# Kernel tuning notes

Measured on AMD Instinct MI355X. Metric: run time of the kernel, lower is better.

## Reference

```python
import jax, jax.numpy as jnp
import numpy as np

N_NODES = 50000
N_EDGES = 800000
N_GRAPHS = 256
C_FEAT = 108
MLP_DIM = 88
OUT_DIM = 100


def setup_inputs() -> dict:
    key = jax.random.key(0)
    ks = jax.random.split(key, 12)
    x = jax.random.normal(ks[0], (N_NODES, C_FEAT), dtype=jnp.float32)
    edge_index = jax.random.randint(ks[1], (2, N_EDGES), 0, N_NODES, dtype=jnp.int64)
    batch = jnp.sort(jax.random.randint(ks[2], (N_NODES,), 0, N_GRAPHS, dtype=jnp.int64))

    def glorot(k, shape):
        fan_in, fan_out = shape
        s = jnp.sqrt(2.0 / (fan_in + fan_out))
        return jax.random.normal(k, shape, dtype=jnp.float32) * s

    return {
        "x": x,
        "edge_index": edge_index,
        "batch": batch,
        # SAGEConv layer 1: lin_l (neighbors, has bias), lin_r (root, no bias)
        "W1l": glorot(ks[3], (C_FEAT, MLP_DIM)),
        "W1r": glorot(ks[4], (C_FEAT, MLP_DIM)),
        "b1": jnp.zeros((MLP_DIM,), jnp.float32),
        "W2l": glorot(ks[5], (MLP_DIM, MLP_DIM)),
        "W2r": glorot(ks[6], (MLP_DIM, MLP_DIM)),
        "b2": jnp.zeros((MLP_DIM,), jnp.float32),
        "W3l": glorot(ks[7], (MLP_DIM, MLP_DIM)),
        "W3r": glorot(ks[8], (MLP_DIM, MLP_DIM)),
        "b3": jnp.zeros((MLP_DIM,), jnp.float32),
        "Wlin": glorot(ks[9], (MLP_DIM, OUT_DIM)),
        "blin": jnp.zeros((OUT_DIM,), jnp.float32),
    }


def _sage_conv(x, src, dst, Wl, Wr, b):
    """PyG SAGEConv(aggr='mean'): out = lin_l(mean_j x_j) + lin_r(x)."""
    n = x.shape[0]
    msg = x[src]  # [E, d] gather from source nodes
    agg = jax.ops.segment_sum(msg, dst, num_segments=n)  # [N, d]
    cnt = jax.ops.segment_sum(jnp.ones((src.shape[0],), x.dtype), dst, num_segments=n)
    agg = agg / jnp.maximum(cnt, 1.0)[:, None]  # scatter-mean
    return agg @ Wl + b + x @ Wr


def reference(x, edge_index, batch, W1l, W1r, b1, W2l, W2r, b2, W3l, W3r, b3, Wlin, blin):
    src, dst = edge_index[0], edge_index[1]
    h = jax.nn.relu(_sage_conv(x, src, dst, W1l, W1r, b1))
    h = jax.nn.relu(_sage_conv(h, src, dst, W2l, W2r, b2))
    h = jax.nn.relu(_sage_conv(h, src, dst, W3l, W3r, b3))
    pooled = jax.ops.segment_sum(h, batch, num_segments=N_GRAPHS)  # global_add_pool
    return pooled @ Wlin + blin  # [n_graphs, 100]
```

## Files before the change

kernel.cpp:

```cpp
#include <hip/hip_runtime.h>
#include <hip/hip_fp16.h>

#define NN 50000
#define NG 256
#define CF 108
#define MD 88
#define OD 100
#define F2 44
#define HP 96
#define HP2 48
#define YLS 96
#define K1P 128
#define NSB 196
#define SBCAP 5120
#define TILE 2048
#define NCH 12

typedef _Float16 f16x8 __attribute__((ext_vector_type(8)));
typedef float f32x4 __attribute__((ext_vector_type(4)));


__global__ __launch_bounds__(256) void bin_kernel(const int* __restrict__ edge, int E,
                                                  int* __restrict__ sbcur,
                                                  unsigned* __restrict__ sbrec) {
    __shared__ int bcnt[NSB], boff[NSB], bfill[NSB], gbase[NSB];
    __shared__ int sc[256];
    __shared__ unsigned stag[TILE];
    __shared__ unsigned char stagbin[TILE];
    const int tid = threadIdx.x;
    const int t0  = blockIdx.x * TILE;
    const int tcnt = min(TILE, E - t0);

    for (int i = tid; i < NSB; i += 256) bcnt[i] = 0;
    __syncthreads();

    unsigned recs[TILE / 256];
    int      bins[TILE / 256];
    #pragma unroll
    for (int j = 0; j < TILE / 256; ++j) {
        const int e = t0 + j * 256 + tid;
        bins[j] = -1;
        if (e < E) {
            const int dst = edge[E + e], src = edge[e];
            bins[j] = dst >> 8;
            recs[j] = ((unsigned)src << 8) | (unsigned)(dst & 255);
            atomicAdd(&bcnt[bins[j]], 1);
        }
    }
    __syncthreads();

    sc[tid] = (tid < NSB) ? bcnt[tid] : 0;
    __syncthreads();
    for (int d = 1; d < 256; d <<= 1) {
        int v = (tid >= d) ? sc[tid - d] : 0;
        __syncthreads();
        sc[tid] += v;
        __syncthreads();
    }
    if (tid < NSB) {
        boff[tid]  = sc[tid] - bcnt[tid];
        bfill[tid] = sc[tid] - bcnt[tid];
        if (bcnt[tid] > 0) gbase[tid] = atomicAdd(&sbcur[tid], bcnt[tid]);
    }
    __syncthreads();

    #pragma unroll
    for (int j = 0; j < TILE / 256; ++j) {
        if (bins[j] >= 0) {
            int pos = atomicAdd(&bfill[bins[j]], 1);
            stag[pos]    = recs[j];
            stagbin[pos] = (unsigned char)bins[j];
        }
    }
    __syncthreads();

    for (int i = tid; i < tcnt; i += 256) {
        const int b   = stagbin[i];
        const int rel = i - boff[b];
        const int gp  = gbase[b] + rel;
        if (gp < SBCAP) sbrec[(size_t)b * SBCAP + gp] = stag[i];
    }
}


__global__ __launch_bounds__(256) void csr256_kernel(const unsigned* __restrict__ sbrec,
                                                     const int* __restrict__ sbcur,
                                                     int* __restrict__ csr,
                                                     int2* __restrict__ off2, int N) {
    __shared__ int hist[256], base[256], offc[256], sc[256];
    const int b = blockIdx.x, tid = threadIdx.x;
    const int cnt = min(sbcur[b], SBCAP);
    const unsigned* rec = sbrec + (size_t)b * SBCAP;

    hist[tid] = 0;
    __syncthreads();
    for (int r = tid; r < cnt; r += 256) atomicAdd(&hist[rec[r] & 255u], 1);
    __syncthreads();

    sc[tid] = hist[tid];
    __syncthreads();
    for (int d = 1; d < 256; d <<= 1) {
        int v = (tid >= d) ? sc[tid - d] : 0;
        __syncthreads();
        sc[tid] += v;
        __syncthreads();
    }
    base[tid] = sc[tid] - hist[tid];
    offc[tid] = base[tid];
    __syncthreads();

    for (int r = tid; r < cnt; r += 256) {
        const unsigned u = rec[r];
        const int dl = (int)(u & 255u);
        const int pos = atomicAdd(&offc[dl], 1);
        csr[(size_t)b * SBCAP + pos] = (int)(u >> 8);
    }
    __syncthreads();

    const int n = b * 256 + tid;
    if (n < N) off2[n] = make_int2(b * SBCAP + base[tid], hist[tid]);
}


__global__ void convx_kernel(const float* __restrict__ x, _Float16* __restrict__ xh, int N) {
    int i = blockIdx.x * blockDim.x + threadIdx.x;
    if (i >= N * K1P) return;
    int n = i >> 7, k = i & (K1P - 1);
    xh[i] = (k < CF) ? (_Float16)x[n * CF + k] : (_Float16)0.f;
}


__global__ void build_wct_all(const float* __restrict__ W1l, const float* __restrict__ W1r,
                              const float* __restrict__ W2l, const float* __restrict__ W2r,
                              const float* __restrict__ W3l, const float* __restrict__ W3r,
                              _Float16* __restrict__ Wct1, _Float16* __restrict__ Wct23) {
    const int n1 = 176 * K1P;
    const int n2 = 176 * HP;
    int idx = blockIdx.x * blockDim.x + threadIdx.x;
    if (idx < n1) {
        int c = idx / K1P, k = idx - c * K1P;
        float v = (k < CF) ? ((c < MD) ? W1l[k * MD + c] : W1r[k * MD + (c - MD)]) : 0.f;
        Wct1[idx] = (_Float16)v;
    } else if (idx < n1 + 2 * n2) {
        int j = idx - n1;
        const float* Wl = (j < n2) ? W2l : W3l;
        const float* Wr = (j < n2) ? W2r : W3r;
        int jj = (j < n2) ? j : j - n2;
        int c = jj / HP, k = jj - c * HP;
        float v = (k < MD) ? ((c < MD) ? Wl[k * MD + c] : Wr[k * MD + (c - MD)]) : 0.f;
        Wct23[j] = (_Float16)v;
    }
}


template <int KPAD>
__global__ __launch_bounds__(256) void gemm_mfma_kernel(const _Float16* __restrict__ Ah,
                                                        const _Float16* __restrict__ Wct,
                                                        const float* __restrict__ bias,
                                                        _Float16* __restrict__ yl,
                                                        _Float16* __restrict__ yr, int N) {
    const int wave = threadIdx.x >> 6;
    const int lane = threadIdx.x & 63;
    const int r16  = lane & 15;
    const int kg   = lane >> 4;
    const int rbase = blockIdx.x * 128 + wave * 16;

    const int arow0 = min(rbase + r16, N - 1);
    const int arow1 = min(rbase + 64 + r16, N - 1);
    const _Float16* ap0 = Ah + (size_t)arow0 * KPAD + kg * 8;
    const _Float16* ap1 = Ah + (size_t)arow1 * KPAD + kg * 8;

    f32x4 acc[2][11];
    #pragma unroll
    for (int q = 0; q < 2; ++q)
        #pragma unroll
        for (int t = 0; t < 11; ++t) acc[q][t] = (f32x4){0.f, 0.f, 0.f, 0.f};

    #pragma unroll
    for (int ks = 0; ks < KPAD / 32; ++ks) {
        f16x8 af0 = *(const f16x8*)(ap0 + ks * 32);
        f16x8 af1 = *(const f16x8*)(ap1 + ks * 32);
        #pragma unroll
        for (int t = 0; t < 11; ++t) {
            const _Float16* bp = Wct + (size_t)(t * 16 + r16) * KPAD + ks * 32 + kg * 8;
            f16x8 bf = *(const f16x8*)bp;
            acc[0][t] = __builtin_amdgcn_mfma_f32_16x16x32_f16(af0, bf, acc[0][t], 0, 0, 0);
            acc[1][t] = __builtin_amdgcn_mfma_f32_16x16x32_f16(af1, bf, acc[1][t], 0, 0, 0);
        }
    }

    #pragma unroll
    for (int q = 0; q < 2; ++q) {
        const int orow0 = rbase + q * 64 + kg * 4;
        #pragma unroll
        for (int t = 0; t < 11; ++t) {
            const int c = t * 16 + r16;
            const bool isr = (c >= MD);
            const float bv = isr ? bias[c - MD] : 0.f;
            _Float16* dst = isr ? (yr + (c - MD)) : (yl + c);
            const int st = isr ? MD : YLS;
            #pragma unroll
            for (int r = 0; r < 4; ++r) {
                const int row = orow0 + r;
                if (row < N) dst[(size_t)row * st] = (_Float16)(acc[q][t][r] + bv);
            }
        }
    }
}


__global__ void agg_kernel(const _Float16* __restrict__ yl, const _Float16* __restrict__ yr,
                           const int2* __restrict__ off2, const int* __restrict__ csr,
                           _Float16* __restrict__ h, int N) {
    int idx = blockIdx.x * blockDim.x + threadIdx.x;
    if (idx >= N * NCH) return;
    int n = idx / NCH;
    int c = idx - n * NCH;
    if (c >= 11) {
        *(f16x8*)(h + (size_t)n * HP + 88) = (f16x8)(_Float16)0.f;
        return;
    }
    const int2 o = off2[n];
    const int s = o.x, e = o.x + o.y;
    float a0[8] = {0,0,0,0,0,0,0,0}, a1[8] = {0,0,0,0,0,0,0,0};
    float a2[8] = {0,0,0,0,0,0,0,0}, a3[8] = {0,0,0,0,0,0,0,0};
    const size_t cof = (size_t)c * 8;
    int i = s;
    for (; i + 7 < e; i += 8) {
        f16x8 v0 = *(const f16x8*)(yl + (size_t)csr[i]     * YLS + cof);
        f16x8 v1 = *(const f16x8*)(yl + (size_t)csr[i + 1] * YLS + cof);
        f16x8 v2 = *(const f16x8*)(yl + (size_t)csr[i + 2] * YLS + cof);
        f16x8 v3 = *(const f16x8*)(yl + (size_t)csr[i + 3] * YLS + cof);
        f16x8 v4 = *(const f16x8*)(yl + (size_t)csr[i + 4] * YLS + cof);
        f16x8 v5 = *(const f16x8*)(yl + (size_t)csr[i + 5] * YLS + cof);
        f16x8 v6 = *(const f16x8*)(yl + (size_t)csr[i + 6] * YLS + cof);
        f16x8 v7 = *(const f16x8*)(yl + (size_t)csr[i + 7] * YLS + cof);
        #pragma unroll
        for (int j = 0; j < 8; ++j) {
            a0[j] += (float)v0[j] + (float)v1[j];
            a1[j] += (float)v2[j] + (float)v3[j];
            a2[j] += (float)v4[j] + (float)v5[j];
            a3[j] += (float)v6[j] + (float)v7[j];
        }
    }
    for (; i + 1 < e; i += 2) {
        f16x8 v0 = *(const f16x8*)(yl + (size_t)csr[i]     * YLS + cof);
        f16x8 v1 = *(const f16x8*)(yl + (size_t)csr[i + 1] * YLS + cof);
        #pragma unroll
        for (int j = 0; j < 8; ++j) {
            a0[j] += (float)v0[j];
            a1[j] += (float)v1[j];
        }
    }
    if (i < e) {
        f16x8 v0 = *(const f16x8*)(yl + (size_t)csr[i] * YLS + cof);
        #pragma unroll
        for (int j = 0; j < 8; ++j) a0[j] += (float)v0[j];
    }
    const float inv = 1.0f / (float)max(o.y, 1);
    const f16x8 r = *(const f16x8*)(yr + (size_t)n * MD + cof);
    f16x8 outv;
    #pragma unroll
    for (int j = 0; j < 8; ++j) {
        float v = (a0[j] + a1[j] + a2[j] + a3[j]) * inv + (float)r[j];
        outv[j] = (_Float16)fmaxf(v, 0.f);
    }
    *(f16x8*)(h + (size_t)n * HP + cof) = outv;
}


__global__ __launch_bounds__(256) void pool_final_kernel(const __half2* __restrict__ h2,
                                                         const int* __restrict__ batch,
                                                         const float* __restrict__ Wlin,
                                                         const float* __restrict__ blin,
                                                         float* __restrict__ out, int N) {
    __shared__ float red[4][F2][2];
    __shared__ float pooled[MD];
    __shared__ int range[2];
    const int g    = blockIdx.x;
    const int tid  = threadIdx.x;
    const int w    = tid >> 6;
    const int lane = tid & 63;

    if (tid < 2) {
        const int tgt = g + tid;
        int lo = 0, hi = N;
        while (lo < hi) {
            int mid = (lo + hi) >> 1;
            if (batch[mid] < tgt) lo = mid + 1; else hi = mid;
        }
        range[tid] = lo;
    }
    __syncthreads();
    const int s = range[0], e = range[1];

    float ax0 = 0.f, ay0 = 0.f, ax1 = 0.f, ay1 = 0.f;
    if (lane < F2) {
        int n = s + w;
        for (; n + 4 < e; n += 8) {
            __half2 v0 = h2[(size_t)n * HP2 + lane];
            __half2 v1 = h2[(size_t)(n + 4) * HP2 + lane];
            ax0 += __low2float(v0); ay0 += __high2float(v0);
            ax1 += __low2float(v1); ay1 += __high2float(v1);
        }
        if (n < e) {
            __half2 v0 = h2[(size_t)n * HP2 + lane];
            ax0 += __low2float(v0); ay0 += __high2float(v0);
        }
        red[w][lane][0] = ax0 + ax1;
        red[w][lane][1] = ay0 + ay1;
    }
    __syncthreads();
    if (tid < F2) {
        pooled[2 * tid]     = red[0][tid][0] + red[1][tid][0] + red[2][tid][0] + red[3][tid][0];
        pooled[2 * tid + 1] = red[0][tid][1] + red[1][tid][1] + red[2][tid][1] + red[3][tid][1];
    }
    __syncthreads();
    if (tid < OD) {
        float acc = blin[tid];
        #pragma unroll 8
        for (int f = 0; f < MD; ++f)
            acc = fmaf(pooled[f], Wlin[f * OD + tid], acc);
        out[(size_t)g * OD + tid] = acc;
    }
}


extern "C" void kernel_launch(void* const* d_in, const int* in_sizes, int n_in,
                              void* d_out, int out_size, void* d_ws, size_t ws_size,
                              hipStream_t stream) {
    const float* x     = (const float*)d_in[0];
    const int*   edge  = (const int*)d_in[1];
    const int*   batch = (const int*)d_in[2];
    const float* W1l = (const float*)d_in[3];
    const float* W1r = (const float*)d_in[4];
    const float* b1  = (const float*)d_in[5];
    const float* W2l = (const float*)d_in[6];
    const float* W2r = (const float*)d_in[7];
    const float* b2  = (const float*)d_in[8];
    const float* W3l = (const float*)d_in[9];
    const float* W3r = (const float*)d_in[10];
    const float* b3  = (const float*)d_in[11];
    const float* Wlin = (const float*)d_in[12];
    const float* blin = (const float*)d_in[13];
    float* out = (float*)d_out;

    const int N = in_sizes[0] / CF;
    const int E = in_sizes[1] / 2;

    char* ws = (char*)d_ws;
    auto alloc = [&](size_t bytes) -> void* {
        void* p = (void*)ws;
        ws += (bytes + 255) & ~(size_t)255;
        return p;
    };
    int*       sbcur   = (int*)alloc((size_t)NSB * 4);
    unsigned*  sbrec   = (unsigned*)alloc((size_t)NSB * SBCAP * 4);
    int*       csr     = (int*)alloc((size_t)NSB * SBCAP * 4);
    int2*      off2    = (int2*)alloc((size_t)N * 8);
    _Float16*  Wct1    = (_Float16*)alloc((size_t)176 * K1P * 2);
    _Float16*  Wct23   = (_Float16*)alloc((size_t)2 * 176 * HP * 2);
    _Float16*  xh      = (_Float16*)alloc((size_t)N * K1P * 2);
    _Float16*  yl      = (_Float16*)alloc((size_t)N * YLS * 2);
    _Float16*  yr      = (_Float16*)alloc((size_t)N * MD * 2);
    _Float16*  h       = (_Float16*)alloc((size_t)N * HP * 2);

    hipMemsetAsync(sbcur, 0, (size_t)NSB * 4, stream);
    bin_kernel<<<(E + TILE - 1) / TILE, 256, 0, stream>>>(edge, E, sbcur, sbrec);
    csr256_kernel<<<NSB, 256, 0, stream>>>(sbrec, sbcur, csr, off2, N);

    convx_kernel<<<(N * K1P + 255) / 256, 256, 0, stream>>>(x, xh, N);
    build_wct_all<<<(176 * K1P + 2 * 176 * HP + 255) / 256, 256, 0, stream>>>(
        W1l, W1r, W2l, W2r, W3l, W3r, Wct1, Wct23);

    const int gemm_blocks = (N + 127) / 128;
    const int agg_blocks  = (N * NCH + 255) / 256;

    gemm_mfma_kernel<K1P><<<gemm_blocks, 256, 0, stream>>>(xh, Wct1, b1, yl, yr, N);
    agg_kernel<<<agg_blocks, 256, 0, stream>>>(yl, yr, off2, csr, h, N);

    gemm_mfma_kernel<HP><<<gemm_blocks, 256, 0, stream>>>(h, Wct23, b2, yl, yr, N);
    agg_kernel<<<agg_blocks, 256, 0, stream>>>(yl, yr, off2, csr, h, N);

    gemm_mfma_kernel<HP><<<gemm_blocks, 256, 0, stream>>>(h, Wct23 + (size_t)176 * HP, b3, yl, yr, N);
    agg_kernel<<<agg_blocks, 256, 0, stream>>>(yl, yr, off2, csr, h, N);

    pool_final_kernel<<<NG, 256, 0, stream>>>((const __half2*)h, batch, Wlin, blin, out, N);
}
```

Before: 209.4 us.

## Sort nodes by degree for aggregation and merge prep kernels into one launch

The CSR build kernel now counting-sorts each 256-node bucket by in-degree (capped at 63) and writes a node order array. The aggregation kernels walk nodes in that order, so threads in a wave handle similar-degree nodes, which reduces divergence from uneven loop trip counts. Binning, input conversion and weight transpose are also fused into one prep kernel to save launches. The cost is an extra indirection per thread, scattered writes to h, and some padded slots that return early.

```diff
diff --git a/kernel.cpp b/kernel.cpp
--- a/kernel.cpp
+++ b/kernel.cpp
@@ -20,65 +20,99 @@
 typedef float f32x4 __attribute__((ext_vector_type(4)));
 
 
-__global__ __launch_bounds__(256) void bin_kernel(const int* __restrict__ edge, int E,
-                                                  int* __restrict__ sbcur,
-                                                  unsigned* __restrict__ sbrec) {
-    __shared__ int bcnt[NSB], boff[NSB], bfill[NSB], gbase[NSB];
-    __shared__ int sc[256];
-    __shared__ unsigned stag[TILE];
-    __shared__ unsigned char stagbin[TILE];
+__global__ __launch_bounds__(256) void prep_kernel(const int* __restrict__ edge, int E,
+                                                   int* __restrict__ sbcur,
+                                                   unsigned* __restrict__ sbrec,
+                                                   const float* __restrict__ x,
+                                                   _Float16* __restrict__ xh, int N,
+                                                   const float* __restrict__ W1l, const float* __restrict__ W1r,
+                                                   const float* __restrict__ W2l, const float* __restrict__ W2r,
+                                                   const float* __restrict__ W3l, const float* __restrict__ W3r,
+                                                   _Float16* __restrict__ Wct1, _Float16* __restrict__ Wct23,
+                                                   int nbin, int nconvx) {
     const int tid = threadIdx.x;
-    const int t0  = blockIdx.x * TILE;
-    const int tcnt = min(TILE, E - t0);
-
-    for (int i = tid; i < NSB; i += 256) bcnt[i] = 0;
-    __syncthreads();
-
-    unsigned recs[TILE / 256];
-    int      bins[TILE / 256];
-    #pragma unroll
-    for (int j = 0; j < TILE / 256; ++j) {
-        const int e = t0 + j * 256 + tid;
-        bins[j] = -1;
-        if (e < E) {
-            const int dst = edge[E + e], src = edge[e];
-            bins[j] = dst >> 8;
-            recs[j] = ((unsigned)src << 8) | (unsigned)(dst & 255);
-            atomicAdd(&bcnt[bins[j]], 1);
-        }
-    }
-    __syncthreads();
-
-    sc[tid] = (tid < NSB) ? bcnt[tid] : 0;
-    __syncthreads();
-    for (int d = 1; d < 256; d <<= 1) {
-        int v = (tid >= d) ? sc[tid - d] : 0;
-        __syncthreads();
-        sc[tid] += v;
-        __syncthreads();
-    }
-    if (tid < NSB) {
-        boff[tid]  = sc[tid] - bcnt[tid];
-        bfill[tid] = sc[tid] - bcnt[tid];
-        if (bcnt[tid] > 0) gbase[tid] = atomicAdd(&sbcur[tid], bcnt[tid]);
-    }
-    __syncthreads();
-
-    #pragma unroll
-    for (int j = 0; j < TILE / 256; ++j) {
-        if (bins[j] >= 0) {
-            int pos = atomicAdd(&bfill[bins[j]], 1);
-            stag[pos]    = recs[j];
-            stagbin[pos] = (unsigned char)bins[j];
-        }
-    }
-    __syncthreads();
-
-    for (int i = tid; i < tcnt; i += 256) {
-        const int b   = stagbin[i];
-        const int rel = i - boff[b];
-        const int gp  = gbase[b] + rel;
-        if (gp < SBCAP) sbrec[(size_t)b * SBCAP + gp] = stag[i];
+    const int bb  = blockIdx.x;
+
+    if (bb < nbin) {
+        __shared__ int bcnt[NSB], boff[NSB], bfill[NSB], gbase[NSB];
+        __shared__ int sc[256];
+        __shared__ unsigned stag[TILE];
+        __shared__ unsigned char stagbin[TILE];
+        const int t0  = bb * TILE;
+        const int tcnt = min(TILE, E - t0);
+
+        for (int i = tid; i < NSB; i += 256) bcnt[i] = 0;
+        __syncthreads();
+
+        unsigned recs[TILE / 256];
+        int      bins[TILE / 256];
+        #pragma unroll
+        for (int j = 0; j < TILE / 256; ++j) {
+            const int e = t0 + j * 256 + tid;
+            bins[j] = -1;
+            if (e < E) {
+                const int dst = edge[E + e], src = edge[e];
+                bins[j] = dst >> 8;
+                recs[j] = ((unsigned)src << 8) | (unsigned)(dst & 255);
+                atomicAdd(&bcnt[bins[j]], 1);
+            }
+        }
+        __syncthreads();
+
+        sc[tid] = (tid < NSB) ? bcnt[tid] : 0;
+        __syncthreads();
+        for (int d = 1; d < 256; d <<= 1) {
+            int v = (tid >= d) ? sc[tid - d] : 0;
+            __syncthreads();
+            sc[tid] += v;
+            __syncthreads();
+        }
+        if (tid < NSB) {
+            boff[tid]  = sc[tid] - bcnt[tid];
+            bfill[tid] = sc[tid] - bcnt[tid];
+            if (bcnt[tid] > 0) gbase[tid] = atomicAdd(&sbcur[tid], bcnt[tid]);
+        }
+        __syncthreads();
+
+        #pragma unroll
+        for (int j = 0; j < TILE / 256; ++j) {
+            if (bins[j] >= 0) {
+                int pos = atomicAdd(&bfill[bins[j]], 1);
+                stag[pos]    = recs[j];
+                stagbin[pos] = (unsigned char)bins[j];
+            }
+        }
+        __syncthreads();
+
+        for (int i = tid; i < tcnt; i += 256) {
+            const int b   = stagbin[i];
+            const int rel = i - boff[b];
+            const int gp  = gbase[b] + rel;
+            if (gp < SBCAP) sbrec[(size_t)b * SBCAP + gp] = stag[i];
+        }
+    } else if (bb < nbin + nconvx) {
+        const int i = (bb - nbin) * 256 + tid;
+        if (i < N * K1P) {
+            int n = i >> 7, k = i & (K1P - 1);
+            xh[i] = (k < CF) ? (_Float16)x[n * CF + k] : (_Float16)0.f;
+        }
+    } else {
+        const int n1 = 176 * K1P;
+        const int n2 = 176 * HP;
+        const int idx = (bb - nbin - nconvx) * 256 + tid;
+        if (idx < n1) {
+            int c = idx / K1P, k = idx - c * K1P;
+            float v = (k < CF) ? ((c < MD) ? W1l[k * MD + c] : W1r[k * MD + (c - MD)]) : 0.f;
+            Wct1[idx] = (_Float16)v;
+        } else if (idx < n1 + 2 * n2) {
+            int j = idx - n1;
+            const float* Wl = (j < n2) ? W2l : W3l;
+            const float* Wr = (j < n2) ? W2r : W3r;
+            int jj = (j < n2) ? j : j - n2;
+            int c = jj / HP, k = jj - c * HP;
+            float v = (k < MD) ? ((c < MD) ? Wl[k * MD + c] : Wr[k * MD + (c - MD)]) : 0.f;
+            Wct23[j] = (_Float16)v;
+        }
     }
 }
 
@@ -86,13 +120,16 @@
 __global__ __launch_bounds__(256) void csr256_kernel(const unsigned* __restrict__ sbrec,
                                                      const int* __restrict__ sbcur,
                                                      int* __restrict__ csr,
-                                                     int2* __restrict__ off2, int N) {
+                                                     int2* __restrict__ off2,
+                                                     int* __restrict__ order, int N) {
     __shared__ int hist[256], base[256], offc[256], sc[256];
+    __shared__ int dcnt[64], dpos[64];
     const int b = blockIdx.x, tid = threadIdx.x;
     const int cnt = min(sbcur[b], SBCAP);
     const unsigned* rec = sbrec + (size_t)b * SBCAP;
 
     hist[tid] = 0;
+    if (tid < 64) dcnt[tid] = 0;
     __syncthreads();
     for (int r = tid; r < cnt; r += 256) atomicAdd(&hist[rec[r] & 255u], 1);
     __syncthreads();
@@ -115,41 +152,26 @@
         const int pos = atomicAdd(&offc[dl], 1);
         csr[(size_t)b * SBCAP + pos] = (int)(u >> 8);
     }
-    __syncthreads();
 
     const int n = b * 256 + tid;
+    const int deg = (n < N) ? min(hist[tid], 63) : 63;
+    atomicAdd(&dcnt[deg], 1);
+    __syncthreads();
+    if (tid < 64) {
+        int v = dcnt[tid];
+        int incl = v;
+        #pragma unroll
+        for (int s = 1; s < 64; s <<= 1) {
+            int t = __shfl_up(incl, s, 64);
+            if (tid >= s) incl += t;
+        }
+        dpos[tid] = incl - v;
+    }
+    __syncthreads();
+    const int rank = atomicAdd(&dpos[deg], 1);
+    order[b * 256 + rank] = (n < N) ? n : -1;
+
     if (n < N) off2[n] = make_int2(b * SBCAP + base[tid], hist[tid]);
-}
-
-
-__global__ void convx_kernel(const float* __restrict__ x, _Float16* __restrict__ xh, int N) {
-    int i = blockIdx.x * blockDim.x + threadIdx.x;
-    if (i >= N * K1P) return;
-    int n = i >> 7, k = i & (K1P - 1);
-    xh[i] = (k < CF) ? (_Float16)x[n * CF + k] : (_Float16)0.f;
-}
-
-
-__global__ void build_wct_all(const float* __restrict__ W1l, const float* __restrict__ W1r,
-                              const float* __restrict__ W2l, const float* __restrict__ W2r,
-                              const float* __restrict__ W3l, const float* __restrict__ W3r,
-                              _Float16* __restrict__ Wct1, _Float16* __restrict__ Wct23) {
-    const int n1 = 176 * K1P;
-    const int n2 = 176 * HP;
-    int idx = blockIdx.x * blockDim.x + threadIdx.x;
-    if (idx < n1) {
-        int c = idx / K1P, k = idx - c * K1P;
-        float v = (k < CF) ? ((c < MD) ? W1l[k * MD + c] : W1r[k * MD + (c - MD)]) : 0.f;
-        Wct1[idx] = (_Float16)v;
-    } else if (idx < n1 + 2 * n2) {
-        int j = idx - n1;
-        const float* Wl = (j < n2) ? W2l : W3l;
-        const float* Wr = (j < n2) ? W2r : W3r;
-        int jj = (j < n2) ? j : j - n2;
-        int c = jj / HP, k = jj - c * HP;
-        float v = (k < MD) ? ((c < MD) ? Wl[k * MD + c] : Wr[k * MD + (c - MD)]) : 0.f;
-        Wct23[j] = (_Float16)v;
-    }
 }
 
 
@@ -211,11 +233,14 @@
 
 __global__ void agg_kernel(const _Float16* __restrict__ yl, const _Float16* __restrict__ yr,
                            const int2* __restrict__ off2, const int* __restrict__ csr,
-                           _Float16* __restrict__ h, int N) {
+                           const int* __restrict__ order,
+                           _Float16* __restrict__ h, int total) {
     int idx = blockIdx.x * blockDim.x + threadIdx.x;
-    if (idx >= N * NCH) return;
-    int n = idx / NCH;
-    int c = idx - n * NCH;
+    if (idx >= total) return;
+    int slot = idx / NCH;
+    int c = idx - slot * NCH;
+    const int n = order[slot];
+    if (n < 0) return;
     if (c >= 11) {
         *(f16x8*)(h + (size_t)n * HP + 88) = (f16x8)(_Float16)0.f;
         return;
@@ -358,6 +383,7 @@
     unsigned*  sbrec   = (unsigned*)alloc((size_t)NSB * SBCAP * 4);
     int*       csr     = (int*)alloc((size_t)NSB * SBCAP * 4);
     int2*      off2    = (int2*)alloc((size_t)N * 8);
+    int*       order   = (int*)alloc((size_t)NSB * 256 * 4);
     _Float16*  Wct1    = (_Float16*)alloc((size_t)176 * K1P * 2);
     _Float16*  Wct23   = (_Float16*)alloc((size_t)2 * 176 * HP * 2);
     _Float16*  xh      = (_Float16*)alloc((size_t)N * K1P * 2);
@@ -365,25 +391,28 @@
     _Float16*  yr      = (_Float16*)alloc((size_t)N * MD * 2);
     _Float16*  h       = (_Float16*)alloc((size_t)N * HP * 2);
 
+    const int nbin   = (E + TILE - 1) / TILE;
+    const int nconvx = (N * K1P + 255) / 256;
+    const int nwct   = (176 * K1P + 2 * 176 * HP + 255) / 256;
+
     hipMemsetAsync(sbcur, 0, (size_t)NSB * 4, stream);
-    bin_kernel<<<(E + TILE - 1) / TILE, 256, 0, stream>>>(edge, E, sbcur, sbrec);
-    csr256_kernel<<<NSB, 256, 0, stream>>>(sbrec, sbcur, csr, off2, N);
-
-    convx_kernel<<<(N * K1P + 255) / 256, 256, 0, stream>>>(x, xh, N);
-    build_wct_all<<<(176 * K1P + 2 * 176 * HP + 255) / 256, 256, 0, stream>>>(
-        W1l, W1r, W2l, W2r, W3l, W3r, Wct1, Wct23);
+    prep_kernel<<<nbin + nconvx + nwct, 256, 0, stream>>>(
+        edge, E, sbcur, sbrec, x, xh, N,
+        W1l, W1r, W2l, W2r, W3l, W3r, Wct1, Wct23, nbin, nconvx);
+    csr256_kernel<<<NSB, 256, 0, stream>>>(sbrec, sbcur, csr, off2, order, N);
 
     const int gemm_blocks = (N + 127) / 128;
-    const int agg_blocks  = (N * NCH + 255) / 256;
+    const int agg_total   = NSB * 256 * NCH;
+    const int agg_blocks  = (agg_total + 255) / 256;
 
     gemm_mfma_kernel<K1P><<<gemm_blocks, 256, 0, stream>>>(xh, Wct1, b1, yl, yr, N);
-    agg_kernel<<<agg_blocks, 256, 0, stream>>>(yl, yr, off2, csr, h, N);
+    agg_kernel<<<agg_blocks, 256, 0, stream>>>(yl, yr, off2, csr, order, h, agg_total);
 
     gemm_mfma_kernel<HP><<<gemm_blocks, 256, 0, stream>>>(h, Wct23, b2, yl, yr, N);
-    agg_kernel<<<agg_blocks, 256, 0, stream>>>(yl, yr, off2, csr, h, N);
+    agg_kernel<<<agg_blocks, 256, 0, stream>>>(yl, yr, off2, csr, order, h, agg_total);
 
     gemm_mfma_kernel<HP><<<gemm_blocks, 256, 0, stream>>>(h, Wct23 + (size_t)176 * HP, b3, yl, yr, N);
-    agg_kernel<<<agg_blocks, 256, 0, stream>>>(yl, yr, off2, csr, h, N);
+    agg_kernel<<<agg_blocks, 256, 0, stream>>>(yl, yr, off2, csr, order, h, agg_total);
 
     pool_final_kernel<<<NG, 256, 0, stream>>>((const __half2*)h, batch, Wlin, blin, out, N);
 }
```

New measurement: 203.0 us. -3.0%, faster.
